# Performance work log

Measured on AMD Instinct MI355X. Metric: run time of the kernel, lower is better.

## Reference

```python
import jax, jax.numpy as jnp
import numpy as np

B, S, D, OUT, CLS = 131072, 14, 16, 128, 7
EPS = 1e-5
SCALING = 1.0


def _layer_norm(x, g, b):
    # torch LayerNorm over last dim, biased variance
    m = jnp.mean(x, axis=-1, keepdims=True)
    v = jnp.mean((x - m) ** 2, axis=-1, keepdims=True)
    return (x - m) * jax.lax.rsqrt(v + EPS) * g + b


def setup_inputs() -> dict:
    key = jax.random.key(0)
    ks = jax.random.split(key, 20)
    p = lambda k, shp: jax.random.normal(k, shp, dtype=jnp.float32) * 0.05
    inp = {
        "sample": jax.random.normal(ks[0], (B, S, D), dtype=jnp.float32),
        # affine LayerNorms on state(query)/stored(key)/pattern-projection(value) inputs
        "ln_q_g": jnp.ones((D,), jnp.float32), "ln_q_b": jnp.zeros((D,), jnp.float32),
        "ln_k_g": jnp.ones((D,), jnp.float32), "ln_k_b": jnp.zeros((D,), jnp.float32),
        "ln_v_g": jnp.ones((D,), jnp.float32), "ln_v_b": jnp.zeros((D,), jnp.float32),
        # Hopfield association core projections (num_heads=1, head_dim=16)
        "Wq": p(ks[1], (D, D)), "bq": p(ks[2], (D,)),
        "Wk": p(ks[3], (D, D)), "bk": p(ks[4], (D,)),
        "Wv": p(ks[5], (D, D)), "bv": p(ks[6], (D,)),
        # Hopfield output projection 16 -> 128
        "Wo": p(ks[7], (OUT, D)), "bo": p(ks[8], (OUT,)),
        # Linear_m: 14 -> 1
        "Wm": p(ks[9], (1, S)), "bm": p(ks[10], (1,)),
        # Linear_b: 128 -> 7
        "Wb": p(ks[11], (CLS, OUT)), "bb": p(ks[12], (CLS,)),
    }
    return inp


def reference(sample, ln_q_g, ln_q_b, ln_k_g, ln_k_b, ln_v_g, ln_v_b,
              Wq, bq, Wk, bk, Wv, bv, Wo, bo, Wm, bm, Wb, bb):
    # --- Hopfield self-association (single update step) ---
    q_in = _layer_norm(sample, ln_q_g, ln_q_b)   # state pattern
    k_in = _layer_norm(sample, ln_k_g, ln_k_b)   # stored pattern
    v_in = _layer_norm(sample, ln_v_g, ln_v_b)   # pattern projection
    Q = jnp.einsum('bsd,ed->bse', q_in, Wq) + bq  # (B,S,16)
    K = jnp.einsum('bsd,ed->bse', k_in, Wk) + bk
    V = jnp.einsum('bsd,ed->bse', v_in, Wv) + bv
    A = jax.nn.softmax(SCALING * jnp.einsum('bqd,bkd->bqk', Q, K), axis=-1)  # (B,S,S)
    O = jnp.einsum('bqk,bkd->bqd', A, V)          # (B,S,16)
    x = jnp.einsum('bsd,od->bso', O, Wo) + bo     # (B,S,128)
    # --- head: transpose, Linear_m over seq dim, transpose, Linear_b ---
    x = jnp.swapaxes(x, 1, 2)                     # (B,128,S)
    y = jnp.einsum('bos,ms->bom', x, Wm) + bm     # (B,128,1)
    y = jnp.swapaxes(y, 1, 2)                     # (B,1,128)
    z = jnp.einsum('bmo,co->bmc', y, Wb) + bb     # (B,1,7)
    return jax.nn.softmax(z, axis=-1)
```

## Files before the change

kernel.cpp:

```cpp
#include <hip/hip_runtime.h>


#define NBATCH 131072

typedef float    f32x4 __attribute__((ext_vector_type(4)));
typedef _Float16 f16x4 __attribute__((ext_vector_type(4)));
typedef __fp16   h16x2 __attribute__((ext_vector_type(2)));

#define ROR(x,N) __int_as_float(__builtin_amdgcn_update_dpp(0, __float_as_int(x), 0x120 + (N), 0xF, 0xF, false))

static __device__ __forceinline__ f16x4 cvt4(float a, float b, float c, float d) {
    union { f16x4 v; h16x2 h[2]; } u;
    u.h[0] = __builtin_amdgcn_cvt_pkrtz(a, b);
    u.h[1] = __builtin_amdgcn_cvt_pkrtz(c, d);
    return u.v;
}

static __device__ __forceinline__ f32x4 mfma16(f16x4 a, f16x4 b, f32x4 c) {
#if __has_builtin(__builtin_amdgcn_mfma_f32_16x16x16f16)
    return __builtin_amdgcn_mfma_f32_16x16x16f16(a, b, c, 0, 0, 0);
#else
    f32x4 d;
    asm("v_mfma_f32_16x16x16_f16 %0, %1, %2, %3" : "=v"(d) : "v"(a), "v"(b), "v"(c));
    return d;
#endif
}

__global__ __launch_bounds__(256) void hop_prep(
    const float* __restrict__ gq, const float* __restrict__ bq_ln,
    const float* __restrict__ gk,
    const float* __restrict__ gv, const float* __restrict__ bv_ln,
    const float* __restrict__ Wq, const float* __restrict__ bq,
    const float* __restrict__ Wk,
    const float* __restrict__ Wv, const float* __restrict__ bv,
    const float* __restrict__ Wo, const float* __restrict__ bo,
    const float* __restrict__ Wm, const float* __restrict__ bm,
    const float* __restrict__ Wb, const float* __restrict__ bb,
    float* __restrict__ ws)
{
    const float L2E = 1.4426950408889634f;
    __shared__ float WqP[256], WkP[256], WvP[256];
    __shared__ float bqP[16], bvP[16], WcS[112];
    const int t = threadIdx.x;
    {
        const int d = t & 15;
        WqP[t] = Wq[t] * gq[d];
        WkP[t] = Wk[t] * gk[d];
        WvP[t] = Wv[t] * gv[d];
    }
    if (t < 16) {
        float a = bq[t], c = bv[t];
        for (int d = 0; d < 16; ++d) {
            a = fmaf(Wq[t*16+d], bq_ln[d], a);
            c = fmaf(Wv[t*16+d], bv_ln[d], c);
        }
        bqP[t] = a; bvP[t] = c;
    }
    if (t < 112) {
        const int c = t >> 4, e = t & 15;
        float s = 0.f;
        for (int o = 0; o < 128; ++o) s = fmaf(Wb[c*128+o], Wo[o*16+e], s);
        WcS[t] = s;
    }
    __syncthreads();
    {
        const int dd = t >> 4, d = t & 15;
        float m = 0.f;
        for (int e = 0; e < 16; ++e) m = fmaf(WqP[e*16+d], WkP[e*16+dd], m);
        ws[t] = m * L2E;
    }
    if (t < 16) {
        float rr = 0.f;
        for (int e = 0; e < 16; ++e) rr = fmaf(bqP[e], WkP[e*16+t], rr);
        ws[256 + t] = rr * L2E;
    }
    {
        const int c = t >> 4, d = t & 15;
        float s = 0.f;
        if (c < 7)
            for (int e = 0; e < 16; ++e) s = fmaf(WcS[c*16+e], WvP[e*16+d], s);
        ws[272 + t] = s;
    }
    if (t < 16) {
        float v = 0.f;
        if (t < 7) {
            float wmsum = 0.f;
            for (int s = 0; s < 14; ++s) wmsum += Wm[s];
            float s1 = 0.f;
            for (int e = 0; e < 16; ++e) s1 = fmaf(WcS[t*16+e], bvP[e], s1);
            float s2 = 0.f, s3 = 0.f;
            for (int o = 0; o < 128; ++o) { s2 = fmaf(Wb[t*128+o], bo[o], s2); s3 += Wb[t*128+o]; }
            v = wmsum*s1 + wmsum*s2 + bm[0]*s3 + bb[t];
        }
        ws[528 + t] = v * L2E;
        ws[544 + t] = (t < 14) ? Wm[t] * L2E : 0.0f;
    }
}

__global__ __launch_bounds__(256, 8) void hop_main(const float* __restrict__ smp,
                                                   const float* __restrict__ W,
                                                   float* __restrict__ out)
{
    const int wave = (blockIdx.x * 256 + threadIdx.x) >> 6;
    const int l    = threadIdx.x & 63;
    const int col  = l & 15;
    const int q    = l >> 4;

    const float4 mt  = *reinterpret_cast<const float4*>(W + col*16 + q*4);
    const float4 w2  = *reinterpret_cast<const float4*>(W + 272 + col*16 + q*4);
    const float4 r4  = *reinterpret_cast<const float4*>(W + 256 + q*4);
    const float4 wm4 = *reinterpret_cast<const float4*>(W + 544 + q*4);
    const float  c2_l = W[528 + col];
    const f16x4 mtA  = cvt4(mt.x, mt.y, mt.z, mt.w);
    const f16x4 w2B  = cvt4(w2.x, w2.y, w2.z, w2.w);
    const f16x4 ONE  = {(_Float16)1.0f, (_Float16)1.0f, (_Float16)1.0f, (_Float16)1.0f};
    const f16x4 SIXT = {(_Float16)0.0625f, (_Float16)0.0625f, (_Float16)0.0625f, (_Float16)0.0625f};
    const f32x4 zero = {0.f, 0.f, 0.f, 0.f};
    const f32x4 rC   = {r4.x, r4.y, r4.z, r4.w};
    const f32x4 c2C  = {c2_l, c2_l, c2_l, c2_l};
    const bool  hi   = (q == 3);

    const int srow = (col < 14) ? col : 13;
    const float* p0 = smp + (size_t)wave * 896 + srow * 16 + q * 4;
    float* op = out + ((size_t)wave * 4 + q) * 7 + col;

    auto zbatch = [&](const f32x4& x) -> float {
        const f16x4 xf  = cvt4(x[0], x[1], x[2], x[3]);
        const f16x4 xqf = cvt4(x[0]*x[0], x[1]*x[1], x[2]*x[2], x[3]*x[3]);
        const f32x4 S1 = mfma16(SIXT, xf,  zero);
        const f32x4 S2 = mfma16(SIXT, xqf, zero);
        const float mean = S1[0];
        const float var  = fmaf(-mean, mean, S2[0]);
        const float rstd = __builtin_amdgcn_rsqf(var + 1e-5f);
        const float nmr  = -mean * rstd;
        const f16x4 xhA = cvt4(fmaf(x[0], rstd, nmr), fmaf(x[1], rstd, nmr),
                               fmaf(x[2], rstd, nmr), fmaf(x[3], rstd, nmr));
        const f32x4 P = mfma16(xhA, w2B, zero);
        const f32x4 T  = mfma16(mtA, xhA, rC);
        const f16x4 B2 = cvt4(T[0], T[1], T[2], T[3]);
        const f32x4 SS = mfma16(xhA, B2, zero);
        const float e0 = __builtin_amdgcn_exp2f(SS[0]);
        const float e1 = __builtin_amdgcn_exp2f(SS[1]);
        const float e2 = hi ? 0.0f : __builtin_amdgcn_exp2f(SS[2]);
        const float e3 = hi ? 0.0f : __builtin_amdgcn_exp2f(SS[3]);
        const f16x4 E  = cvt4(e0, e1, e2, e3);
        const f16x4 Pf = cvt4(P[0], P[1], P[2], P[3]);
        const f32x4 Zt = mfma16(E, ONE, zero);
        const f32x4 G  = mfma16(E, Pf,  zero);
        const float w0 = wm4.x * __builtin_amdgcn_rcpf(Zt[0]);
        const float w1 = wm4.y * __builtin_amdgcn_rcpf(Zt[1]);
        const float w2s = wm4.z * __builtin_amdgcn_rcpf(Zt[2]);
        const float w3 = wm4.w * __builtin_amdgcn_rcpf(Zt[3]);
        const f16x4 wA = cvt4(w0, w1, w2s, w3);
        const f16x4 Gf = cvt4(G[0], G[1], G[2], G[3]);
        const f32x4 ZZ = mfma16(wA, Gf, c2C);
        return ZZ[0];
    };

    const f32x4 a0 = __builtin_nontemporal_load(reinterpret_cast<const f32x4*>(p0));
    const f32x4 a1 = __builtin_nontemporal_load(reinterpret_cast<const f32x4*>(p0 + 224));
    const f32x4 a2 = __builtin_nontemporal_load(reinterpret_cast<const f32x4*>(p0 + 448));
    const f32x4 a3 = __builtin_nontemporal_load(reinterpret_cast<const f32x4*>(p0 + 672));

    const float z0 = zbatch(a0);
    __builtin_amdgcn_sched_barrier(0);
    const float z1 = zbatch(a1);
    __builtin_amdgcn_sched_barrier(0);
    const float z2 = zbatch(a2);
    __builtin_amdgcn_sched_barrier(0);
    const float z3 = zbatch(a3);

    float z = (q == 1) ? z1 : z0;
    z = (q == 2) ? z2 : z;
    z = (q == 3) ? z3 : z;
    float e = (col < 7) ? __builtin_amdgcn_exp2f(z) : 0.0f;
    float s = e;
    s += ROR(s, 1); s += ROR(s, 2); s += ROR(s, 4); s += ROR(s, 8);
    if (col < 7) __builtin_nontemporal_store(e * __builtin_amdgcn_rcpf(s), op);
}

extern "C" void kernel_launch(void* const* d_in, const int* in_sizes, int n_in,
                              void* d_out, int out_size, void* d_ws, size_t ws_size,
                              hipStream_t stream) {
    (void)in_sizes; (void)n_in; (void)out_size; (void)ws_size;
    const float* smp = (const float*)d_in[0];
    float* ws = (float*)d_ws;
    hop_prep<<<1, 256, 0, stream>>>(
        (const float*)d_in[1],  (const float*)d_in[2],
        (const float*)d_in[3],
        (const float*)d_in[5],  (const float*)d_in[6],
        (const float*)d_in[7],  (const float*)d_in[8],
        (const float*)d_in[9],
        (const float*)d_in[11], (const float*)d_in[12],
        (const float*)d_in[13], (const float*)d_in[14],
        (const float*)d_in[15], (const float*)d_in[16],
        (const float*)d_in[17], (const float*)d_in[18],
        ws);
    hop_main<<<NBATCH * 16 / 256, 256, 0, stream>>>(smp, ws, (float*)d_out);
}
```

Measured before the change: 31.58 us.

## Stage sample tiles into LDS via async global_load_lds, eight samples per wave

```diff
diff --git a/kernel.cpp b/kernel.cpp
--- a/kernel.cpp
+++ b/kernel.cpp
@@ -2,6 +2,8 @@
 
 
 #define NBATCH 131072
+#define NWAVE  16384
+#define NBLK   (NWAVE / 4)
 
 typedef float    f32x4 __attribute__((ext_vector_type(4)));
 typedef _Float16 f16x4 __attribute__((ext_vector_type(4)));
@@ -101,7 +103,9 @@
                                                    const float* __restrict__ W,
                                                    float* __restrict__ out)
 {
+    __shared__ __align__(16) char lds[4 * 7168];
     const int wave = (blockIdx.x * 256 + threadIdx.x) >> 6;
+    const int wsl  = threadIdx.x >> 6;
     const int l    = threadIdx.x & 63;
     const int col  = l & 15;
     const int q    = l >> 4;
@@ -121,10 +125,32 @@
     const bool  hi   = (q == 3);
 
     const int srow = (col < 14) ? col : 13;
-    const float* p0 = smp + (size_t)wave * 896 + srow * 16 + q * 4;
-    float* op = out + ((size_t)wave * 4 + q) * 7 + col;
-
-    auto zbatch = [&](const f32x4& x) -> float {
+    char* lw = lds + wsl * 7168;
+    const int ldsoff = (q * 14 + srow) * 16;
+
+    int off[7];
+    #pragma unroll
+    for (int j = 0; j < 7; ++j) {
+        const int p   = j * 64 + l;
+        const int b   = p / 56;
+        const int rem = p - b * 56;
+        const int qq  = rem / 14;
+        const int rr  = rem - qq * 14;
+        off[j] = b * 896 + rr * 64 + qq * 16;
+    }
+    const char* gw = reinterpret_cast<const char*>(smp) + (size_t)wave * 7168;
+
+    asm volatile("s_waitcnt vmcnt(0)" ::: "memory");
+    #pragma unroll
+    for (int j = 0; j < 7; ++j) {
+        __builtin_amdgcn_global_load_lds(
+            (const __attribute__((address_space(1))) void*)(gw + off[j]),
+            (__attribute__((address_space(3))) void*)(lw + j * 1024),
+            16, 0, 0);
+    }
+
+    auto zbatch = [&](int b) -> float {
+        const f32x4 x = *reinterpret_cast<const f32x4*>(lw + b * 896 + ldsoff);
         const f16x4 xf  = cvt4(x[0], x[1], x[2], x[3]);
         const f16x4 xqf = cvt4(x[0]*x[0], x[1]*x[1], x[2]*x[2], x[3]*x[3]);
         const f32x4 S1 = mfma16(SIXT, xf,  zero);
@@ -157,26 +183,36 @@
         return ZZ[0];
     };
 
-    const f32x4 a0 = __builtin_nontemporal_load(reinterpret_cast<const f32x4*>(p0));
-    const f32x4 a1 = __builtin_nontemporal_load(reinterpret_cast<const f32x4*>(p0 + 224));
-    const f32x4 a2 = __builtin_nontemporal_load(reinterpret_cast<const f32x4*>(p0 + 448));
-    const f32x4 a3 = __builtin_nontemporal_load(reinterpret_cast<const f32x4*>(p0 + 672));
-
-    const float z0 = zbatch(a0);
-    __builtin_amdgcn_sched_barrier(0);
-    const float z1 = zbatch(a1);
-    __builtin_amdgcn_sched_barrier(0);
-    const float z2 = zbatch(a2);
-    __builtin_amdgcn_sched_barrier(0);
-    const float z3 = zbatch(a3);
-
-    float z = (q == 1) ? z1 : z0;
-    z = (q == 2) ? z2 : z;
-    z = (q == 3) ? z3 : z;
-    float e = (col < 7) ? __builtin_amdgcn_exp2f(z) : 0.0f;
-    float s = e;
-    s += ROR(s, 1); s += ROR(s, 2); s += ROR(s, 4); s += ROR(s, 8);
-    if (col < 7) __builtin_nontemporal_store(e * __builtin_amdgcn_rcpf(s), op);
+    asm volatile("s_waitcnt vmcnt(3)" ::: "memory");
+    const float z0 = zbatch(0);
+    __builtin_amdgcn_sched_barrier(0);
+    const float z1 = zbatch(1);
+    __builtin_amdgcn_sched_barrier(0);
+    const float z2 = zbatch(2);
+    __builtin_amdgcn_sched_barrier(0);
+    const float z3 = zbatch(3);
+    asm volatile("s_waitcnt vmcnt(0)" ::: "memory");
+    const float z4 = zbatch(4);
+    __builtin_amdgcn_sched_barrier(0);
+    const float z5 = zbatch(5);
+    __builtin_amdgcn_sched_barrier(0);
+    const float z6 = zbatch(6);
+    __builtin_amdgcn_sched_barrier(0);
+    const float z7 = zbatch(7);
+
+    auto epilogue = [&](float a0, float a1, float a2, float a3, float* o) {
+        float z = (q == 1) ? a1 : a0;
+        z = (q == 2) ? a2 : z;
+        z = (q == 3) ? a3 : z;
+        float e = (col < 7) ? __builtin_amdgcn_exp2f(z) : 0.0f;
+        float s = e;
+        s += ROR(s, 1); s += ROR(s, 2); s += ROR(s, 4); s += ROR(s, 8);
+        if (col < 7) *o = e * __builtin_amdgcn_rcpf(s);
+    };
+    float* ob = out + ((size_t)wave * 8 + q) * 7 + col;
+    epilogue(z0, z1, z2, z3, ob);
+    epilogue(z4, z5, z6, z7, ob + 28);
+
 }
 
 extern "C" void kernel_launch(void* const* d_in, const int* in_sizes, int n_in,
@@ -196,5 +232,5 @@
         (const float*)d_in[15], (const float*)d_in[16],
         (const float*)d_in[17], (const float*)d_in[18],
         ws);
-    hop_main<<<NBATCH * 16 / 256, 256, 0, stream>>>(smp, ws, (float*)d_out);
-}
+    hop_main<<<NBLK, 256, 0, stream>>>(smp, ws, (float*)d_out);
+}
```

After: 40.61 us. 1.29x slower.

## Replace reduction MFMAs with cross-lane shuffles and stagger batch loads

Applied to the files above, without the earlier changes.

```diff
diff --git a/kernel.cpp b/kernel.cpp
--- a/kernel.cpp
+++ b/kernel.cpp
@@ -106,31 +106,27 @@
     const int col  = l & 15;
     const int q    = l >> 4;
 
-    const float4 mt  = *reinterpret_cast<const float4*>(W + col*16 + q*4);
-    const float4 w2  = *reinterpret_cast<const float4*>(W + 272 + col*16 + q*4);
-    const float4 r4  = *reinterpret_cast<const float4*>(W + 256 + q*4);
-    const float4 wm4 = *reinterpret_cast<const float4*>(W + 544 + q*4);
-    const float  c2_l = W[528 + col];
+    const float4 mt = *reinterpret_cast<const float4*>(W + col*16 + q*4);
+    const float4 w2 = *reinterpret_cast<const float4*>(W + 272 + col*16 + q*4);
+    const float4 r4 = *reinterpret_cast<const float4*>(W + 256 + q*4);
+    const float wm_l = W[544 + col];
+    const float c2_l = W[528 + col];
     const f16x4 mtA  = cvt4(mt.x, mt.y, mt.z, mt.w);
     const f16x4 w2B  = cvt4(w2.x, w2.y, w2.z, w2.w);
-    const f16x4 ONE  = {(_Float16)1.0f, (_Float16)1.0f, (_Float16)1.0f, (_Float16)1.0f};
-    const f16x4 SIXT = {(_Float16)0.0625f, (_Float16)0.0625f, (_Float16)0.0625f, (_Float16)0.0625f};
+    const f32x4 rC   = {r4.x, r4.y, r4.z, r4.w};
     const f32x4 zero = {0.f, 0.f, 0.f, 0.f};
-    const f32x4 rC   = {r4.x, r4.y, r4.z, r4.w};
-    const f32x4 c2C  = {c2_l, c2_l, c2_l, c2_l};
     const bool  hi   = (q == 3);
 
     const int srow = (col < 14) ? col : 13;
     const float* p0 = smp + (size_t)wave * 896 + srow * 16 + q * 4;
-    float* op = out + ((size_t)wave * 4 + q) * 7 + col;
 
     auto zbatch = [&](const f32x4& x) -> float {
-        const f16x4 xf  = cvt4(x[0], x[1], x[2], x[3]);
-        const f16x4 xqf = cvt4(x[0]*x[0], x[1]*x[1], x[2]*x[2], x[3]*x[3]);
-        const f32x4 S1 = mfma16(SIXT, xf,  zero);
-        const f32x4 S2 = mfma16(SIXT, xqf, zero);
-        const float mean = S1[0];
-        const float var  = fmaf(-mean, mean, S2[0]);
+        float s1 = (x[0] + x[1]) + (x[2] + x[3]);
+        float s2 = fmaf(x[0], x[0], fmaf(x[1], x[1], fmaf(x[2], x[2], x[3]*x[3])));
+        s1 += __shfl_xor(s1, 16, 64);  s2 += __shfl_xor(s2, 16, 64);
+        s1 += __shfl_xor(s1, 32, 64);  s2 += __shfl_xor(s2, 32, 64);
+        const float mean = s1 * 0.0625f;
+        const float var  = fmaf(s2, 0.0625f, -mean * mean);
         const float rstd = __builtin_amdgcn_rsqf(var + 1e-5f);
         const float nmr  = -mean * rstd;
         const f16x4 xhA = cvt4(fmaf(x[0], rstd, nmr), fmaf(x[1], rstd, nmr),
@@ -143,32 +139,30 @@
         const float e1 = __builtin_amdgcn_exp2f(SS[1]);
         const float e2 = hi ? 0.0f : __builtin_amdgcn_exp2f(SS[2]);
         const float e3 = hi ? 0.0f : __builtin_amdgcn_exp2f(SS[3]);
-        const f16x4 E  = cvt4(e0, e1, e2, e3);
-        const f16x4 Pf = cvt4(P[0], P[1], P[2], P[3]);
-        const f32x4 Zt = mfma16(E, ONE, zero);
-        const f32x4 G  = mfma16(E, Pf,  zero);
-        const float w0 = wm4.x * __builtin_amdgcn_rcpf(Zt[0]);
-        const float w1 = wm4.y * __builtin_amdgcn_rcpf(Zt[1]);
-        const float w2s = wm4.z * __builtin_amdgcn_rcpf(Zt[2]);
-        const float w3 = wm4.w * __builtin_amdgcn_rcpf(Zt[3]);
-        const f16x4 wA = cvt4(w0, w1, w2s, w3);
-        const f16x4 Gf = cvt4(G[0], G[1], G[2], G[3]);
-        const f32x4 ZZ = mfma16(wA, Gf, c2C);
-        return ZZ[0];
+        float Z = (e0 + e1) + (e2 + e3);
+        Z += __shfl_xor(Z, 16, 64);
+        Z += __shfl_xor(Z, 32, 64);
+        const float f = wm_l * __builtin_amdgcn_rcpf(Z);
+        const f16x4 EfA = cvt4(e0*f, e1*f, e2*f, e3*f);
+        const f16x4 Pf  = cvt4(P[0], P[1], P[2], P[3]);
+        const f32x4 G = mfma16(EfA, Pf, zero);
+        float zz = (G[0] + G[1]) + (G[2] + G[3]);
+        zz += __shfl_xor(zz, 16, 64);
+        zz += __shfl_xor(zz, 32, 64);
+        return zz + c2_l;
     };
 
-    const f32x4 a0 = __builtin_nontemporal_load(reinterpret_cast<const f32x4*>(p0));
-    const f32x4 a1 = __builtin_nontemporal_load(reinterpret_cast<const f32x4*>(p0 + 224));
-    const f32x4 a2 = __builtin_nontemporal_load(reinterpret_cast<const f32x4*>(p0 + 448));
-    const f32x4 a3 = __builtin_nontemporal_load(reinterpret_cast<const f32x4*>(p0 + 672));
-
-    const float z0 = zbatch(a0);
+    const f32x4 x0 = __builtin_nontemporal_load(reinterpret_cast<const f32x4*>(p0));
+    const f32x4 x1 = __builtin_nontemporal_load(reinterpret_cast<const f32x4*>(p0 + 224));
+    const float z0 = zbatch(x0);
     __builtin_amdgcn_sched_barrier(0);
-    const float z1 = zbatch(a1);
+    const f32x4 x2 = __builtin_nontemporal_load(reinterpret_cast<const f32x4*>(p0 + 448));
+    const float z1 = zbatch(x1);
     __builtin_amdgcn_sched_barrier(0);
-    const float z2 = zbatch(a2);
+    const f32x4 x3 = __builtin_nontemporal_load(reinterpret_cast<const f32x4*>(p0 + 672));
+    const float z2 = zbatch(x2);
     __builtin_amdgcn_sched_barrier(0);
-    const float z3 = zbatch(a3);
+    const float z3 = zbatch(x3);
 
     float z = (q == 1) ? z1 : z0;
     z = (q == 2) ? z2 : z;
@@ -176,7 +170,9 @@
     float e = (col < 7) ? __builtin_amdgcn_exp2f(z) : 0.0f;
     float s = e;
     s += ROR(s, 1); s += ROR(s, 2); s += ROR(s, 4); s += ROR(s, 8);
-    if (col < 7) __builtin_nontemporal_store(e * __builtin_amdgcn_rcpf(s), op);
+    if (col < 7)
+        __builtin_nontemporal_store(e * __builtin_amdgcn_rcpf(s),
+                                    out + ((size_t)wave * 4 + q) * 7 + col);
 }
 
 extern "C" void kernel_launch(void* const* d_in, const int* in_sizes, int n_in,
```

After: 34.05 us. 1.08x slower.
